# Optimization experiments

Hardware: AMD Instinct MI355X
Metric: run time of the kernel (lower is better)

Reference implementation:

```python
import jax, jax.numpy as jnp
import numpy as np

EPS = 1e-8
LN_EPS = 1e-5


def _norm_no_nan(x, axis=-1, keepdims=False):
    return jnp.sqrt(jnp.clip(jnp.sum(x * x, axis=axis, keepdims=keepdims), EPS))


def gvp_apply(s, v, wh, ws_w, ws_b, wv, use_acts):
    # s: [*, si], v: [*, vi, 3]; activations = (relu, sigmoid) when use_acts
    vt = jnp.swapaxes(v, -1, -2)                        # [*, 3, vi]
    vh = jnp.matmul(vt, wh.T)                           # [*, 3, h]
    vn = _norm_no_nan(vh, axis=-2)                      # [*, h]
    s_out = jnp.matmul(jnp.concatenate([s, vn], -1), ws_w.T) + ws_b
    v_out = jnp.swapaxes(jnp.matmul(vh, wv.T), -1, -2)  # [*, vo, 3]
    if use_acts:
        v_out = v_out * jax.nn.sigmoid(_norm_no_nan(v_out, axis=-1, keepdims=True))
        s_out = jax.nn.relu(s_out)
    return s_out, v_out


def tuple_layernorm(s, v, g, b):
    mu = jnp.mean(s, -1, keepdims=True)
    var = jnp.mean(jnp.square(s - mu), -1, keepdims=True)
    s = (s - mu) / jnp.sqrt(var + LN_EPS) * g + b
    vn2 = jnp.clip(jnp.sum(v * v, -1, keepdims=True), EPS)  # [N, nv, 1]
    v = v / jnp.sqrt(jnp.mean(vn2, -2, keepdims=True))
    return s, v


def gvp_conv_layer(node_s, node_v, edge_s, edge_v, edge_index,
                   msg0_wh, msg0_wsw, msg0_wsb, msg0_wv,
                   msg1_wh, msg1_wsw, msg1_wsb, msg1_wv,
                   msg2_wh, msg2_wsw, msg2_wsb, msg2_wv,
                   ln0_g, ln0_b,
                   ff0_wh, ff0_wsw, ff0_wsb, ff0_wv,
                   ff1_wh, ff1_wsw, ff1_wsb, ff1_wv,
                   ln1_g, ln1_b):
    N = node_s.shape[0]
    src, dst = edge_index[0], edge_index[1]  # PyG: x_j = x[edge_index[0]], x_i = x[edge_index[1]]
    # gather + tuple_cat((s_j, v_j), edge_attr, (s_i, v_i))
    ms = jnp.concatenate([node_s[src], edge_s, node_s[dst]], -1)   # [E, 2*ns+es]
    mv = jnp.concatenate([node_v[src], edge_v, node_v[dst]], -2)   # [E, 2*nv+ev, 3]
    # message function: 3 GVPs, last with no activations
    ms, mv = gvp_apply(ms, mv, msg0_wh, msg0_wsw, msg0_wsb, msg0_wv, True)
    ms, mv = gvp_apply(ms, mv, msg1_wh, msg1_wsw, msg1_wsb, msg1_wv, True)
    ms, mv = gvp_apply(ms, mv, msg2_wh, msg2_wsw, msg2_wsb, msg2_wv, False)
    # mean aggregation over incoming edges per target node
    cnt = jax.ops.segment_sum(jnp.ones_like(ms[:, 0]), dst, num_segments=N)
    denom = jnp.maximum(cnt, 1.0)[:, None]
    agg_s = jax.ops.segment_sum(ms, dst, num_segments=N) / denom
    agg_v = jax.ops.segment_sum(mv, dst, num_segments=N) / denom[..., None]
    # residual + LayerNorm (dropout = identity in eval)
    s, v = tuple_layernorm(node_s + agg_s, node_v + agg_v, ln0_g, ln0_b)
    # feedforward: 2 GVPs, hidden (4*ns, 2*nv), last with no activations
    fs, fv = gvp_apply(s, v, ff0_wh, ff0_wsw, ff0_wsb, ff0_wv, True)
    fs, fv = gvp_apply(fs, fv, ff1_wh, ff1_wsw, ff1_wsb, ff1_wv, False)
    return tuple_layernorm(s + fs, v + fv, ln1_g, ln1_b)


def setup_inputs() -> dict:
    key = jax.random.key(0)
    ks = iter(jax.random.split(key, 64))
    N, E = 10000, 200000
    NS, NV, ES, EV = 128, 32, 32, 1

    def _lin(out_d, in_d):
        return jax.random.normal(next(ks), (out_d, in_d), jnp.float32) / np.float32(np.sqrt(in_d))

    inp = {
        'node_s': jax.random.normal(next(ks), (N, NS), jnp.float32),
        'node_v': jax.random.normal(next(ks), (N, NV, 3), jnp.float32),
        'edge_s': jax.random.normal(next(ks), (E, ES), jnp.float32),
        'edge_v': jax.random.normal(next(ks), (E, EV, 3), jnp.float32),
        'edge_index': jax.random.randint(next(ks), (2, E), 0, N, dtype=jnp.int32),
    }
    si0, vi0 = 2 * NS + ES, 2 * NV + EV            # 288, 65
    h0 = max(vi0, NV)                              # 65
    inp['msg0_wh'] = _lin(h0, vi0)
    inp['msg0_wsw'] = _lin(NS, h0 + si0)
    inp['msg0_wsb'] = jnp.zeros((NS,), jnp.float32)
    inp['msg0_wv'] = _lin(NV, h0)
    for name in ('msg1', 'msg2'):
        inp[name + '_wh'] = _lin(NV, NV)
        inp[name + '_wsw'] = _lin(NS, NV + NS)
        inp[name + '_wsb'] = jnp.zeros((NS,), jnp.float32)
        inp[name + '_wv'] = _lin(NV, NV)
    inp['ln0_g'] = jnp.ones((NS,), jnp.float32)
    inp['ln0_b'] = jnp.zeros((NS,), jnp.float32)
    HS, HV = 4 * NS, 2 * NV                        # 512, 64
    hf0 = max(NV, HV)                              # 64
    inp['ff0_wh'] = _lin(hf0, NV)
    inp['ff0_wsw'] = _lin(HS, hf0 + NS)
    inp['ff0_wsb'] = jnp.zeros((HS,), jnp.float32)
    inp['ff0_wv'] = _lin(HV, hf0)
    hf1 = max(HV, NV)                              # 64
    inp['ff1_wh'] = _lin(hf1, HV)
    inp['ff1_wsw'] = _lin(NS, hf1 + HS)
    inp['ff1_wsb'] = jnp.zeros((NS,), jnp.float32)
    inp['ff1_wv'] = _lin(NV, hf1)
    inp['ln1_g'] = jnp.ones((NS,), jnp.float32)
    inp['ln1_b'] = jnp.zeros((NS,), jnp.float32)
    return inp


def reference(node_s, node_v, edge_s, edge_v, edge_index,
              msg0_wh, msg0_wsw, msg0_wsb, msg0_wv,
              msg1_wh, msg1_wsw, msg1_wsb, msg1_wv,
              msg2_wh, msg2_wsw, msg2_wsb, msg2_wv,
              ln0_g, ln0_b,
              ff0_wh, ff0_wsw, ff0_wsb, ff0_wv,
              ff1_wh, ff1_wsw, ff1_wsb, ff1_wv,
              ln1_g, ln1_b):
    return gvp_conv_layer(node_s, node_v, edge_s, edge_v, edge_index,
                          msg0_wh, msg0_wsw, msg0_wsb, msg0_wv,
                          msg1_wh, msg1_wsw, msg1_wsb, msg1_wv,
                          msg2_wh, msg2_wsw, msg2_wsb, msg2_wv,
                          ln0_g, ln0_b,
                          ff0_wh, ff0_wsw, ff0_wsb, ff0_wv,
                          ff1_wh, ff1_wsw, ff1_wsb, ff1_wv,
                          ln1_g, ln1_b)
```

## Files before the change

kernel.cpp:

```cpp
#include <hip/hip_runtime.h>

typedef unsigned short u16;
typedef __attribute__((ext_vector_type(8))) short bf16x8;
typedef __attribute__((ext_vector_type(4))) float f32x4;

__device__ __forceinline__ float b2f(u16 h){ return __uint_as_float(((unsigned)h)<<16); }
__device__ __forceinline__ u16 f2b(float f){
  unsigned u = __float_as_uint(f);
  unsigned r = ((u>>16)&1u) + 0x7fffu;
  return (u16)((u+r)>>16);
}
__device__ __forceinline__ short4 pack4(float4 f){
  short4 s; s.x=(short)f2b(f.x); s.y=(short)f2b(f.y); s.z=(short)f2b(f.z); s.w=(short)f2b(f.w);
  return s;
}

#define WB0   0
#define WB1   49152
#define WB2   69632
#define WBF0  90112
#define WBF1  188416
#define WB_TOTAL 262144

#define V_WH0   0
#define V_WV0   7680
#define V_WH1   10752
#define V_WV1   11776
#define V_WH2   12800
#define V_WV2   13824
#define NV_FF0H 14848
#define NV_FF0V 16896
#define NV_FF1H 20992
#define NV_FF1V 25088
#define WV_TOTAL 27136

__global__ __launch_bounds__(256) void k_wb(const float* __restrict__ w0,
    const float* __restrict__ w1, const float* __restrict__ w2,
    const float* __restrict__ f0, const float* __restrict__ f1,
    u16* __restrict__ WB){
  int t = blockIdx.x*256 + threadIdx.x;
  if (t < 49152){
    int o = t/384, k = t - o*384;
    WB[WB0 + t] = f2b(k < 353 ? w0[(size_t)o*353 + k] : 0.f);
    return;
  }
  t -= 49152;
  if (t < 20480){ WB[WB1 + t] = f2b(w1[t]); return; }
  t -= 20480;
  if (t < 20480){ WB[WB2 + t] = f2b(w2[t]); return; }
  t -= 20480;
  if (t < 98304){ WB[WBF0 + t] = f2b(f0[t]); return; }
  t -= 98304;
  if (t < 73728){ WB[WBF1 + t] = f2b(f1[t]); return; }
}

__global__ __launch_bounds__(256) void k_wv(const float* __restrict__ wh0, const float* __restrict__ wv0,
    const float* __restrict__ wh1, const float* __restrict__ wv1,
    const float* __restrict__ wh2, const float* __restrict__ wv2,
    const float* __restrict__ nf0h, const float* __restrict__ nf0v,
    const float* __restrict__ nf1h, const float* __restrict__ nf1v,
    u16* __restrict__ WVb){
  int t = blockIdx.x*256 + threadIdx.x;
  if (t < 7680){
    int n=t/96, k=t-n*96;
    float v = 0.f;
    if (n < 65){
      if (k < 32)       v = wh0[(size_t)n*65 + k];
      else if (k < 64)  v = wh0[(size_t)n*65 + 33 + (k-32)];
      else if (k == 64) v = wh0[(size_t)n*65 + 32];
    }
    WVb[V_WH0+t] = f2b(v);
    return;
  }
  t -= 7680;
  if (t < 3072){
    int n=t/96, k=t-n*96;
    WVb[V_WV0+t] = f2b((k<65) ? wv0[(size_t)n*65+k] : 0.f);
    return;
  }
  t -= 3072;
  if (t < 1024){ WVb[V_WH1+t]=f2b(wh1[t]); return; }
  t -= 1024;
  if (t < 1024){ WVb[V_WV1+t]=f2b(wv1[t]); return; }
  t -= 1024;
  if (t < 1024){ WVb[V_WH2+t]=f2b(wh2[t]); return; }
  t -= 1024;
  if (t < 1024){ WVb[V_WV2+t]=f2b(wv2[t]); return; }
  t -= 1024;
  if (t < 2048){ WVb[NV_FF0H+t]=f2b(nf0h[t]); return; }
  t -= 2048;
  if (t < 4096){ WVb[NV_FF0V+t]=f2b(nf0v[t]); return; }
  t -= 4096;
  if (t < 4096){ WVb[NV_FF1H+t]=f2b(nf1h[t]); return; }
  t -= 4096;
  if (t < 2048){ WVb[NV_FF1V+t]=f2b(nf1v[t]); return; }
}

__global__ __launch_bounds__(256) void k_prep(const float* __restrict__ node_s,
    const float* __restrict__ node_v, u16* __restrict__ node_sb,
    u16* __restrict__ node_vb, int N){
  int t = blockIdx.x*256 + threadIdx.x;
  if (t < N*128){ node_sb[t] = f2b(node_s[t]); return; }
  t -= N*128;
  if (t < N*96){
    int n=t/96, r=t-n*96, d=r>>5, vo=r&31;
    node_vb[(size_t)n*96 + d*32 + vo] = f2b(node_v[(size_t)n*96 + vo*3 + d]);
  }
}

__global__ __launch_bounds__(256) void k_hist(const int* __restrict__ ei, int E,
                                              float* __restrict__ cnt){
  int e = blockIdx.x*256 + threadIdx.x;
  if (e < E) atomicAdd(&cnt[ei[(size_t)E + e]], 1.f);
}

__global__ __launch_bounds__(256) void k_scan(const float* __restrict__ cnt,
                                              int* __restrict__ wpos, int N){
  __shared__ int part[256];
  const int tid = threadIdx.x;
  const int per = (N + 255)/256;
  const int base = tid*per;
  int s = 0;
  for (int i=0;i<per;++i){ int n=base+i; if (n<N) s += (int)cnt[n]; }
  part[tid] = s; __syncthreads();
  for (int st=1; st<256; st<<=1){
    int v = (tid>=st) ? part[tid-st] : 0;
    __syncthreads();
    part[tid] += v;
    __syncthreads();
  }
  int run = part[tid] - s;
  for (int i=0;i<per;++i){ int n=base+i; if (n<N){ wpos[n]=run; run += (int)cnt[n]; } }
}

__global__ __launch_bounds__(256) void k_scatter(const int* __restrict__ ei, int E,
                                                 int* __restrict__ wpos, int* __restrict__ perm){
  int e = blockIdx.x*256 + threadIdx.x;
  if (e >= E) return;
  int d = ei[(size_t)E + e];
  int pos = atomicAdd(&wpos[d], 1);
  perm[pos] = e;
}

__global__ __launch_bounds__(256) void k_sortedge(
    const float* __restrict__ es, const float* __restrict__ ev,
    const int* __restrict__ perm,
    u16* __restrict__ esb, u16* __restrict__ evb, int E)
{
  int t = blockIdx.x*256 + threadIdx.x;
  if (t >= E*9) return;
  int pos = t/9, p = t - pos*9;
  int e = perm[pos];
  if (p < 8){
    float4 f = *(const float4*)&es[(size_t)e*32 + 4*p];
    *(short4*)&esb[(size_t)pos*32 + 4*p] = pack4(f);
  } else {
    evb[(size_t)pos*4+0] = f2b(ev[(size_t)e*3+0]);
    evb[(size_t)pos*4+1] = f2b(ev[(size_t)e*3+1]);
    evb[(size_t)pos*4+2] = f2b(ev[(size_t)e*3+2]);
    evb[(size_t)pos*4+3] = 0;
  }
}

#define EPB 32
__global__ __launch_bounds__(512) void k_edge_fused(
    const u16* __restrict__ node_sb, const u16* __restrict__ node_vb,
    const u16* __restrict__ esb, const u16* __restrict__ evb,
    const int* __restrict__ ei, int E, const int* __restrict__ perm,
    const u16* __restrict__ WB, const u16* __restrict__ WVb,
    const float* __restrict__ b0p, const float* __restrict__ b1p, const float* __restrict__ b2p,
    float* __restrict__ agg_s, float* __restrict__ agg_v)
{
  __shared__ __align__(16) char R1[42240];
  __shared__ __align__(16) u16 VN0[EPB][80];
  __shared__ __align__(16) u16 VN1[EPB][32];
  __shared__ __align__(16) u16 VN2[EPB][32];
  __shared__ int SD[EPB][2];
  u16 (*B0)[104]  = (u16(*)[104])R1;
  u16 (*B1)[104]  = (u16(*)[104])(R1 + 20480);
  float (*SCv)[33] = (float(*)[33])R1;
  u16 (*A)[392]   = (u16(*)[392])R1;
  float (*SC)[132] = (float(*)[132])R1;

  const int tid = threadIdx.x;
  const int w = tid>>6, l = tid&63;
  const int le0 = blockIdx.x*EPB;

  if (tid < EPB){
    int le = le0 + tid;
    int ge = (le<E) ? perm[le] : 0;
    SD[tid][0] = ei[ge];
    SD[tid][1] = ei[(size_t)E + ge];
  }
  __syncthreads();
  for (int u=tid; u<96*16; u+=512){
    int r=u>>4, g=u&15, ee=r/3, d=r-ee*3;
    int le=le0+ee;
    short4 v = {0,0,0,0};
    if (le<E){
      int node = (g<8) ? SD[ee][0] : SD[ee][1];
      v = *(const short4*)&node_vb[(size_t)node*96 + d*32 + 4*(g&7)];
    }
    *(short4*)&B0[r][4*g] = v;
  }
  for (int u=tid; u<96*8; u+=512){
    int r=u>>3, g=u&7, ee=r/3, d=r-ee*3;
    int le=le0+ee;
    short4 v = {0,0,0,0};
    if (g==0 && le<E) v.x = (short)evb[(size_t)le*4 + d];
    *(short4*)&B0[r][64+4*g] = v;
  }
  for (int u=tid; u<96*4; u+=512){
    int r=u>>2, g=u&3;
    *(short4*)&B1[r][80+4*g] = (short4){0,0,0,0};
  }
  __syncthreads();

  auto mm = [&](const u16 (*Ai)[104], int woff, int Kp, int NT, u16 (*C)[104]){
    const int nks = Kp>>5;
    for (int t=w; t<6*NT; t+=8){
      int mt = t % 6, nt = t / 6;
      f32x4 acc = {0.f,0.f,0.f,0.f};
      for (int ks=0; ks<nks; ++ks){
        bf16x8 af = *(const bf16x8*)&Ai[mt*16 + (l&15)][ks*32 + (l>>4)*8];
        bf16x8 bf = *(const bf16x8*)&WVb[woff + (size_t)(nt*16 + (l&15))*Kp + ks*32 + (l>>4)*8];
        acc = __builtin_amdgcn_mfma_f32_16x16x32_bf16(af, bf, acc, 0, 0, 0);
      }
      const int col = nt*16 + (l&15);
      const int r0 = mt*16 + (l>>4)*4;
      C[r0+0][col]=f2b(acc[0]); C[r0+1][col]=f2b(acc[1]);
      C[r0+2][col]=f2b(acc[2]); C[r0+3][col]=f2b(acc[3]);
    }
  };

  mm(B0, V_WH0, 96, 5, B1);
  __syncthreads();
  for (int u=tid; u<EPB*80; u+=512){
    int ee=u/80, h=u-ee*80;
    u16 val = 0;
    if (h<65){
      float x0=b2f(B1[ee*3+0][h]), x1=b2f(B1[ee*3+1][h]), x2=b2f(B1[ee*3+2][h]);
      val = f2b(sqrtf(fmaxf(x0*x0+x1*x1+x2*x2, 1e-8f)));
    }
    VN0[ee][h] = val;
  }
  mm(B1, V_WV0, 96, 2, B0);
  __syncthreads();
  for (int u=tid; u<EPB*32; u+=512){
    int ee=u>>5, vo=u&31;
    float x0=b2f(B0[ee*3+0][vo]), x1=b2f(B0[ee*3+1][vo]), x2=b2f(B0[ee*3+2][vo]);
    float nn=sqrtf(fmaxf(x0*x0+x1*x1+x2*x2, 1e-8f));
    float sg=1.f/(1.f+__expf(-nn));
    B0[ee*3+0][vo]=f2b(x0*sg); B0[ee*3+1][vo]=f2b(x1*sg); B0[ee*3+2][vo]=f2b(x2*sg);
  }
  __syncthreads();
  mm(B0, V_WH1, 32, 2, B1);
  __syncthreads();
  for (int u=tid; u<EPB*32; u+=512){
    int ee=u>>5, h=u&31;
    float x0=b2f(B1[ee*3+0][h]), x1=b2f(B1[ee*3+1][h]), x2=b2f(B1[ee*3+2][h]);
    VN1[ee][h] = f2b(sqrtf(fmaxf(x0*x0+x1*x1+x2*x2, 1e-8f)));
  }
  mm(B1, V_WV1, 32, 2, B0);
  __syncthreads();
  for (int u=tid; u<EPB*32; u+=512){
    int ee=u>>5, vo=u&31;
    float x0=b2f(B0[ee*3+0][vo]), x1=b2f(B0[ee*3+1][vo]), x2=b2f(B0[ee*3+2][vo]);
    float nn=sqrtf(fmaxf(x0*x0+x1*x1+x2*x2, 1e-8f));
    float sg=1.f/(1.f+__expf(-nn));
    B0[ee*3+0][vo]=f2b(x0*sg); B0[ee*3+1][vo]=f2b(x1*sg); B0[ee*3+2][vo]=f2b(x2*sg);
  }
  __syncthreads();
  mm(B0, V_WH2, 32, 2, B1);
  __syncthreads();
  for (int u=tid; u<EPB*32; u+=512){
    int ee=u>>5, h=u&31;
    float x0=b2f(B1[ee*3+0][h]), x1=b2f(B1[ee*3+1][h]), x2=b2f(B1[ee*3+2][h]);
    VN2[ee][h] = f2b(sqrtf(fmaxf(x0*x0+x1*x1+x2*x2, 1e-8f)));
  }
  for (int t=w; t<12; t+=8){
    int mt = t % 6, nt = t / 6;
    f32x4 acc = {0.f,0.f,0.f,0.f};
    bf16x8 af = *(const bf16x8*)&B1[mt*16 + (l&15)][(l>>4)*8];
    bf16x8 bf = *(const bf16x8*)&WVb[V_WV2 + (size_t)(nt*16 + (l&15))*32 + (l>>4)*8];
    acc = __builtin_amdgcn_mfma_f32_16x16x32_bf16(af, bf, acc, 0, 0, 0);
    const int vo = nt*16 + (l&15);
    const int r0 = mt*16 + (l>>4)*4;
    #pragma unroll
    for (int j=0;j<4;++j){
      int r = r0 + j;
      int le = le0 + r/3;
      SCv[r][vo] = (le < E) ? acc[j] : 0.f;
    }
  }
  __syncthreads();
  if (tid < 96){
    const int vo = tid & 31, d = tid >> 5;
    float run = 0.f; int prev = -1;
    for (int ee=0; ee<EPB; ++ee){
      int le = le0 + ee;
      int dn = (le<E) ? SD[ee][1] : -1;
      if (dn != prev){
        if (prev >= 0) atomicAdd(&agg_v[(size_t)prev*96 + vo*3 + d], run);
        run = 0.f; prev = dn;
      }
      run += SCv[ee*3+d][vo];
    }
    if (prev >= 0) atomicAdd(&agg_v[(size_t)prev*96 + vo*3 + d], run);
  }
  __syncthreads();

  for (int u=tid; u<EPB*98; u+=512){
    int ee = u/98, g = u - ee*98;
    int le = le0+ee;
    short4 v = {0,0,0,0};
    if (le<E){
      if (g < 32)      v = *(const short4*)&node_sb[(size_t)SD[ee][0]*128 + 4*g];
      else if (g < 40) v = *(const short4*)&esb[(size_t)le*32 + 4*(g-32)];
      else if (g < 72) v = *(const short4*)&node_sb[(size_t)SD[ee][1]*128 + 4*(g-40)];
      else if (g < 92) v = *(const short4*)&VN0[ee][4*(g-72)];
    }
    *(short4*)&A[ee][4*g] = v;
  }
  __syncthreads();

  const int mt = w>>2, nt = w&3;
  const int n_a = nt*32 + (l&15), n_b = n_a + 16;
  const int kq = (l>>4)*8;
  const int ma = mt*16 + (l&15);
  f32x4 ca = {0.f,0.f,0.f,0.f}, cb = {0.f,0.f,0.f,0.f};

  for (int kk=0; kk<384; kk+=32){
    bf16x8 af = *(const bf16x8*)&A[ma][kk + kq];
    bf16x8 b1 = *(const bf16x8*)&WB[WB0 + (size_t)n_a*384 + kk + kq];
    bf16x8 b2 = *(const bf16x8*)&WB[WB0 + (size_t)n_b*384 + kk + kq];
    ca = __builtin_amdgcn_mfma_f32_16x16x32_bf16(af, b1, ca, 0, 0, 0);
    cb = __builtin_amdgcn_mfma_f32_16x16x32_bf16(af, b2, cb, 0, 0, 0);
  }
  __syncthreads();
  {
    float ba = b0p[n_a], bb = b0p[n_b];
    #pragma unroll
    for (int j=0;j<4;++j){
      int r = mt*16 + (l>>4)*4 + j;
      A[r][n_a] = f2b(fmaxf(ca[j] + ba, 0.f));
      A[r][n_b] = f2b(fmaxf(cb[j] + bb, 0.f));
    }
  }
  for (int u=tid; u<EPB*8; u+=512){
    int ee=u>>3, q=u&7;
    *(short4*)&A[ee][128+4*q] = *(const short4*)&VN1[ee][4*q];
  }
  __syncthreads();

  ca = (f32x4){0.f,0.f,0.f,0.f}; cb = (f32x4){0.f,0.f,0.f,0.f};
  for (int kk=0; kk<160; kk+=32){
    bf16x8 af = *(const bf16x8*)&A[ma][kk + kq];
    bf16x8 b1 = *(const bf16x8*)&WB[WB1 + (size_t)n_a*160 + kk + kq];
    bf16x8 b2 = *(const bf16x8*)&WB[WB1 + (size_t)n_b*160 + kk + kq];
    ca = __builtin_amdgcn_mfma_f32_16x16x32_bf16(af, b1, ca, 0, 0, 0);
    cb = __builtin_amdgcn_mfma_f32_16x16x32_bf16(af, b2, cb, 0, 0, 0);
  }
  __syncthreads();
  {
    float ba = b1p[n_a], bb = b1p[n_b];
    #pragma unroll
    for (int j=0;j<4;++j){
      int r = mt*16 + (l>>4)*4 + j;
      A[r][n_a] = f2b(fmaxf(ca[j] + ba, 0.f));
      A[r][n_b] = f2b(fmaxf(cb[j] + bb, 0.f));
    }
  }
  for (int u=tid; u<EPB*8; u+=512){
    int ee=u>>3, q=u&7;
    *(short4*)&A[ee][128+4*q] = *(const short4*)&VN2[ee][4*q];
  }
  __syncthreads();

  ca = (f32x4){0.f,0.f,0.f,0.f}; cb = (f32x4){0.f,0.f,0.f,0.f};
  for (int kk=0; kk<160; kk+=32){
    bf16x8 af = *(const bf16x8*)&A[ma][kk + kq];
    bf16x8 b1 = *(const bf16x8*)&WB[WB2 + (size_t)n_a*160 + kk + kq];
    bf16x8 b2 = *(const bf16x8*)&WB[WB2 + (size_t)n_b*160 + kk + kq];
    ca = __builtin_amdgcn_mfma_f32_16x16x32_bf16(af, b1, ca, 0, 0, 0);
    cb = __builtin_amdgcn_mfma_f32_16x16x32_bf16(af, b2, cb, 0, 0, 0);
  }
  __syncthreads();
  {
    float ba = b2p[n_a], bb = b2p[n_b];
    #pragma unroll
    for (int j=0;j<4;++j){
      int r = mt*16 + (l>>4)*4 + j;
      int le = le0 + r;
      SC[r][n_a] = (le<E) ? (ca[j] + ba) : 0.f;
      SC[r][n_b] = (le<E) ? (cb[j] + bb) : 0.f;
    }
  }
  __syncthreads();
  if (tid < 128){
    const int c = tid;
    float run = 0.f; int prev = -1;
    for (int r=0; r<EPB; ++r){
      int le = le0 + r;
      int dn = (le<E) ? SD[r][1] : -1;
      if (dn != prev){
        if (prev >= 0) atomicAdd(&agg_s[(size_t)prev*128 + c], run);
        run = 0.f; prev = dn;
      }
      run += SC[r][c];
    }
    if (prev >= 0) atomicAdd(&agg_s[(size_t)prev*128 + c], run);
  }
}

__global__ __launch_bounds__(256) void k_ln0(
    const float* __restrict__ node_s, const float* __restrict__ node_v,
    const float* __restrict__ agg_s, const float* __restrict__ agg_v,
    const float* __restrict__ cnt,
    const float* __restrict__ g, const float* __restrict__ b,
    float* __restrict__ s_mid, float* __restrict__ v_mid, int N)
{
  const int tid = threadIdx.x, q = tid&3;
  const int n = blockIdx.x*64 + (tid>>2);
  const bool live = n < N;
  const float inv = live ? 1.f/fmaxf(cnt[n], 1.f) : 1.f;
  float xs[32];
  float sum=0.f, ss=0.f;
  if (live){
    #pragma unroll
    for (int j=0;j<8;++j){
      float4 a = *(const float4*)&node_s[(size_t)n*128 + q*32 + 4*j];
      float4 c = *(const float4*)&agg_s[(size_t)n*128 + q*32 + 4*j];
      xs[4*j+0]=a.x+c.x*inv; xs[4*j+1]=a.y+c.y*inv; xs[4*j+2]=a.z+c.z*inv; xs[4*j+3]=a.w+c.w*inv;
      sum += xs[4*j+0]+xs[4*j+1]+xs[4*j+2]+xs[4*j+3];
      ss  += xs[4*j+0]*xs[4*j+0]+xs[4*j+1]*xs[4*j+1]+xs[4*j+2]*xs[4*j+2]+xs[4*j+3]*xs[4*j+3];
    }
  }
  sum += __shfl_xor(sum,1); sum += __shfl_xor(sum,2);
  ss  += __shfl_xor(ss,1);  ss  += __shfl_xor(ss,2);
  const float mu = sum*(1.f/128.f);
  const float var = fmaxf(ss*(1.f/128.f) - mu*mu, 0.f);
  const float rstd = rsqrtf(var + 1e-5f);
  if (live){
    #pragma unroll
    for (int j=0;j<8;++j){
      float4 gg = *(const float4*)&g[q*32 + 4*j];
      float4 bb = *(const float4*)&b[q*32 + 4*j];
      float4 o;
      o.x=(xs[4*j+0]-mu)*rstd*gg.x+bb.x; o.y=(xs[4*j+1]-mu)*rstd*gg.y+bb.y;
      o.z=(xs[4*j+2]-mu)*rstd*gg.z+bb.z; o.w=(xs[4*j+3]-mu)*rstd*gg.w+bb.w;
      *(float4*)&s_mid[(size_t)n*128 + q*32 + 4*j] = o;
    }
  }
  float yv[24]; float vs=0.f;
  if (live){
    #pragma unroll
    for (int j=0;j<6;++j){
      float4 a = *(const float4*)&node_v[(size_t)n*96 + q*24 + 4*j];
      float4 c = *(const float4*)&agg_v[(size_t)n*96 + q*24 + 4*j];
      yv[4*j+0]=a.x+c.x*inv; yv[4*j+1]=a.y+c.y*inv; yv[4*j+2]=a.z+c.z*inv; yv[4*j+3]=a.w+c.w*inv;
    }
    #pragma unroll
    for (int vv=0; vv<8; ++vv){
      float z0=yv[3*vv], z1=yv[3*vv+1], z2=yv[3*vv+2];
      vs += fmaxf(z0*z0+z1*z1+z2*z2, 1e-8f);
    }
  }
  vs += __shfl_xor(vs,1); vs += __shfl_xor(vs,2);
  const float scale = rsqrtf(vs*(1.f/32.f));
  if (live){
    #pragma unroll
    for (int vv=0; vv<8; ++vv){
      int vo = q*8 + vv;
      v_mid[(size_t)n*96 + vo]      = yv[3*vv]*scale;
      v_mid[(size_t)n*96 + 32 + vo] = yv[3*vv+1]*scale;
      v_mid[(size_t)n*96 + 64 + vo] = yv[3*vv+2]*scale;
    }
  }
}

__global__ __launch_bounds__(256) void k_node_v(
    const float* __restrict__ v_mid, const u16* __restrict__ WVb,
    u16* __restrict__ vn0f, u16* __restrict__ vn1f, float* __restrict__ fv1, int N)
{
  __shared__ __align__(16) u16 B0[96][104];
  __shared__ __align__(16) u16 B1[96][104];
  const int tid = threadIdx.x;
  const int w = tid>>6, l = tid&63;
  const int n0 = blockIdx.x*32;

  for (int u=tid; u<96*8; u+=256){
    int r=u>>3, g=u&7, nd=r/3, d=r-nd*3;
    int n=n0+nd;
    short4 v = {0,0,0,0};
    if (n<N) v = pack4(*(const float4*)&v_mid[(size_t)n*96 + d*32 + 4*g]);
    *(short4*)&B0[r][4*g] = v;
  }
  __syncthreads();

  auto mm = [&](const u16 (*A)[104], int woff, int Kp, int NT, u16 (*C)[104]){
    const int nks = Kp>>5;
    for (int t=w; t<6*NT; t+=4){
      int mt = t % 6, nt = t / 6;
      f32x4 acc = {0.f,0.f,0.f,0.f};
      for (int ks=0; ks<nks; ++ks){
        bf16x8 af = *(const bf16x8*)&A[mt*16 + (l&15)][ks*32 + (l>>4)*8];
        bf16x8 bf = *(const bf16x8*)&WVb[woff + (size_t)(nt*16 + (l&15))*Kp + ks*32 + (l>>4)*8];
        acc = __builtin_amdgcn_mfma_f32_16x16x32_bf16(af, bf, acc, 0, 0, 0);
      }
      const int col = nt*16 + (l&15);
      const int r0 = mt*16 + (l>>4)*4;
      C[r0+0][col]=f2b(acc[0]); C[r0+1][col]=f2b(acc[1]);
      C[r0+2][col]=f2b(acc[2]); C[r0+3][col]=f2b(acc[3]);
    }
  };

  mm(B0, NV_FF0H, 32, 4, B1);
  __syncthreads();
  for (int u=tid; u<32*64; u+=256){
    int nd=u>>6, h=u&63;
    int n=n0+nd;
    if (n<N){
      float x0=b2f(B1[nd*3+0][h]), x1=b2f(B1[nd*3+1][h]), x2=b2f(B1[nd*3+2][h]);
      vn0f[(size_t)n*64+h] = f2b(sqrtf(fmaxf(x0*x0+x1*x1+x2*x2, 1e-8f)));
    }
  }
  mm(B1, NV_FF0V, 64, 4, B0);
  __syncthreads();
  for (int u=tid; u<32*64; u+=256){
    int nd=u>>6, vo=u&63;
    float x0=b2f(B0[nd*3+0][vo]), x1=b2f(B0[nd*3+1][vo]), x2=b2f(B0[nd*3+2][vo]);
    float nn=sqrtf(fmaxf(x0*x0+x1*x1+x2*x2, 1e-8f));
    float sg=1.f/(1.f+__expf(-nn));
    B0[nd*3+0][vo]=f2b(x0*sg); B0[nd*3+1][vo]=f2b(x1*sg); B0[nd*3+2][vo]=f2b(x2*sg);
  }
  __syncthreads();
  mm(B0, NV_FF1H, 64, 4, B1);
  __syncthreads();
  for (int u=tid; u<32*64; u+=256){
    int nd=u>>6, h=u&63;
    int n=n0+nd;
    if (n<N){
      float x0=b2f(B1[nd*3+0][h]), x1=b2f(B1[nd*3+1][h]), x2=b2f(B1[nd*3+2][h]);
      vn1f[(size_t)n*64+h] = f2b(sqrtf(fmaxf(x0*x0+x1*x1+x2*x2, 1e-8f)));
    }
  }
  for (int t=w; t<12; t+=4){
    int mt = t % 6, nt = t / 6;
    f32x4 acc = {0.f,0.f,0.f,0.f};
    for (int ks=0; ks<2; ++ks){
      bf16x8 af = *(const bf16x8*)&B1[mt*16 + (l&15)][ks*32 + (l>>4)*8];
      bf16x8 bf = *(const bf16x8*)&WVb[NV_FF1V + (size_t)(nt*16 + (l&15))*64 + ks*32 + (l>>4)*8];
      acc = __builtin_amdgcn_mfma_f32_16x16x32_bf16(af, bf, acc, 0, 0, 0);
    }
    const int vo = nt*16 + (l&15);
    const int r0 = mt*16 + (l>>4)*4;
    #pragma unroll
    for (int j=0;j<4;++j){
      int r = r0 + j;
      int nd = r/3, d = r - nd*3;
      int n = n0 + nd;
      if (n < N) fv1[(size_t)n*96 + d*32 + vo] = acc[j];
    }
  }
}

__global__ __launch_bounds__(512) void k_node_s(
    const float* __restrict__ s_mid, const u16* __restrict__ vn0f, const u16* __restrict__ vn1f,
    const float* __restrict__ v_mid, const float* __restrict__ fv1,
    const u16* __restrict__ WB,
    const float* __restrict__ fb0, const float* __restrict__ fb1,
    const float* __restrict__ ln1g, const float* __restrict__ ln1b,
    float* __restrict__ out, int N)
{
  __shared__ __align__(16) char U1[16896];
  __shared__ __align__(16) u16 A2[32][584];
  u16 (*A1)[200] = (u16(*)[200])U1;
  float (*FS)[132] = (float(*)[132])U1;
  const int tid = threadIdx.x;
  const int n0 = blockIdx.x*32;

  for (int u=tid; u<32*48; u+=512){
    int nd = u/48, g = u - nd*48;
    int n = n0+nd;
    short4 v = {0,0,0,0};
    if (n<N){
      if (g < 32) v = pack4(*(const float4*)&s_mid[(size_t)n*128 + 4*g]);
      else        v = *(const short4*)&vn0f[(size_t)n*64 + 4*(g-32)];
    }
    *(short4*)&A1[nd][4*g] = v;
  }
  __syncthreads();

  const int w = tid>>6, l = tid&63;
  const int mt = w>>2, ng = w&3;
  const int kq = (l>>4)*8;
  const int ma = mt*16 + (l&15);
  const int r0 = mt*16 + (l>>4)*4;

  for (int nt2=0; nt2<8; ++nt2){
    const int nt = ng*8 + nt2;
    const int col = nt*16 + (l&15);
    f32x4 acc = {0.f,0.f,0.f,0.f};
    for (int ks=0; ks<6; ++ks){
      bf16x8 af = *(const bf16x8*)&A1[ma][ks*32 + kq];
      bf16x8 bf = *(const bf16x8*)&WB[WBF0 + (size_t)col*192 + ks*32 + kq];
      acc = __builtin_amdgcn_mfma_f32_16x16x32_bf16(af, bf, acc, 0, 0, 0);
    }
    float bias = fb0[col];
    #pragma unroll
    for (int j=0;j<4;++j) A2[r0+j][col] = f2b(fmaxf(acc[j] + bias, 0.f));
  }
  __syncthreads();
  for (int u=tid; u<32*16; u+=512){
    int nd=u>>4, q=u&15;
    int n=n0+nd;
    short4 v = {0,0,0,0};
    if (n<N) v = *(const short4*)&vn1f[(size_t)n*64 + 4*q];
    *(short4*)&A2[nd][512+4*q] = v;
  }
  __syncthreads();

  for (int nt2=0; nt2<2; ++nt2){
    const int nt = ng*2 + nt2;
    const int col = nt*16 + (l&15);
    f32x4 acc = {0.f,0.f,0.f,0.f};
    for (int ks=0; ks<18; ++ks){
      bf16x8 af = *(const bf16x8*)&A2[ma][ks*32 + kq];
      bf16x8 bf = *(const bf16x8*)&WB[WBF1 + (size_t)col*576 + ks*32 + kq];
      acc = __builtin_amdgcn_mfma_f32_16x16x32_bf16(af, bf, acc, 0, 0, 0);
    }
    float bias = fb1[col];
    #pragma unroll
    for (int j=0;j<4;++j) FS[r0+j][col] = acc[j] + bias;
  }
  __syncthreads();

  {
    const int nd = tid>>4, q = tid&15;
    const int n = n0 + nd;
    const bool live = n < N;
    float xs[8], sum=0.f, ss=0.f;
    #pragma unroll
    for (int j=0;j<8;++j){
      int c = q*8 + j;
      float x = 0.f;
      if (live) x = s_mid[(size_t)n*128 + c] + FS[nd][c];
      xs[j] = x; sum += x; ss += x*x;
    }
    #pragma unroll
    for (int m=1; m<16; m<<=1){ sum += __shfl_xor(sum, m); ss += __shfl_xor(ss, m); }
    const float mu = sum*(1.f/128.f);
    const float var = fmaxf(ss*(1.f/128.f) - mu*mu, 0.f);
    const float rstd = rsqrtf(var + 1e-5f);
    if (live){
      #pragma unroll
      for (int j=0;j<8;++j){
        int c = q*8 + j;
        out[(size_t)n*128 + c] = (xs[j]-mu)*rstd*ln1g[c] + ln1b[c];
      }
    }
    float z[2][3]; float vs = 0.f;
    #pragma unroll
    for (int j=0;j<2;++j){
      int vo = q + 16*j;
      #pragma unroll
      for (int d=0;d<3;++d){
        float y = live ? (v_mid[(size_t)n*96 + d*32 + vo] + fv1[(size_t)n*96 + d*32 + vo]) : 0.f;
        z[j][d] = y;
      }
      vs += fmaxf(z[j][0]*z[j][0]+z[j][1]*z[j][1]+z[j][2]*z[j][2], 1e-8f);
    }
    #pragma unroll
    for (int m=1; m<16; m<<=1) vs += __shfl_xor(vs, m);
    const float scale = rsqrtf(vs*(1.f/32.f));
    if (live){
      size_t base = (size_t)N*128 + (size_t)n*96;
      #pragma unroll
      for (int j=0;j<2;++j){
        int vo = q + 16*j;
        out[base + vo*3 + 0] = z[j][0]*scale;
        out[base + vo*3 + 1] = z[j][1]*scale;
        out[base + vo*3 + 2] = z[j][2]*scale;
      }
    }
  }
}

extern "C" void kernel_launch(void* const* d_in, const int* in_sizes, int n_in,
                              void* d_out, int out_size, void* d_ws, size_t ws_size,
                              hipStream_t stream)
{
  (void)n_in; (void)out_size; (void)ws_size;
  const int N = in_sizes[0]/128;
  const int E = in_sizes[4]/2;
  const int* ei = (const int*)d_in[4];

  size_t off = 0;
  auto alloc = [&](size_t bytes)->char*{
    size_t o = (off + 255) & ~(size_t)255;
    off = o + bytes;
    return (char*)d_ws + o;
  };
  u16*   WB      = (u16*)alloc((size_t)WB_TOTAL*2);
  u16*   WVb     = (u16*)alloc((size_t)WV_TOTAL*2);
  float* agg_s   = (float*)alloc((size_t)N*128*4);
  float* agg_v   = (float*)alloc((size_t)N*96*4);
  float* cnt     = (float*)alloc((size_t)N*4);
  size_t aggBytes = (size_t)((char*)(cnt+N) - (char*)agg_s);
  float* s_mid   = (float*)alloc((size_t)N*128*4);
  float* v_mid   = (float*)alloc((size_t)N*96*4);
  u16*   node_sb = (u16*)alloc((size_t)N*128*2);
  u16*   node_vb = (u16*)alloc((size_t)N*96*2);
  u16*   vn0f    = (u16*)alloc((size_t)N*64*2);
  u16*   vn1f    = (u16*)alloc((size_t)N*64*2);
  float* fv1     = (float*)alloc((size_t)N*96*4);
  int*   wpos    = (int*)alloc((size_t)N*4);
  int*   perm    = (int*)alloc((size_t)E*4);
  u16*   esb     = (u16*)alloc((size_t)E*32*2);
  u16*   evb     = (u16*)alloc((size_t)E*4*2);

  hipMemsetAsync(agg_s, 0, aggBytes, stream);
  k_wb<<<dim3((WB_TOTAL+255)/256), dim3(256), 0, stream>>>(
      (const float*)d_in[6], (const float*)d_in[10], (const float*)d_in[14],
      (const float*)d_in[20], (const float*)d_in[24], WB);
  k_wv<<<dim3((WV_TOTAL+255)/256), dim3(256), 0, stream>>>(
      (const float*)d_in[5], (const float*)d_in[8], (const float*)d_in[9],
      (const float*)d_in[12], (const float*)d_in[13], (const float*)d_in[16],
      (const float*)d_in[19], (const float*)d_in[22], (const float*)d_in[23],
      (const float*)d_in[26], WVb);
  k_prep<<<dim3((N*224+255)/256), dim3(256), 0, stream>>>(
      (const float*)d_in[0], (const float*)d_in[1], node_sb, node_vb, N);
  k_hist<<<dim3((E+255)/256), dim3(256), 0, stream>>>(ei, E, cnt);
  k_scan<<<dim3(1), dim3(256), 0, stream>>>(cnt, wpos, N);
  k_scatter<<<dim3((E+255)/256), dim3(256), 0, stream>>>(ei, E, wpos, perm);
  k_sortedge<<<dim3(((size_t)E*9+255)/256), dim3(256), 0, stream>>>(
      (const float*)d_in[2], (const float*)d_in[3], perm, esb, evb, E);

  k_edge_fused<<<dim3((E+EPB-1)/EPB), dim3(512), 0, stream>>>(
      node_sb, node_vb, esb, evb, ei, E, perm, WB, WVb,
      (const float*)d_in[7], (const float*)d_in[11], (const float*)d_in[15],
      agg_s, agg_v);

  k_ln0<<<dim3((N+63)/64), dim3(256), 0, stream>>>(
      (const float*)d_in[0], (const float*)d_in[1], agg_s, agg_v, cnt,
      (const float*)d_in[17], (const float*)d_in[18], s_mid, v_mid, N);

  k_node_v<<<dim3((N+31)/32), dim3(256), 0, stream>>>(v_mid, WVb, vn0f, vn1f, fv1, N);
  k_node_s<<<dim3((N+31)/32), dim3(512), 0, stream>>>(
      s_mid, vn0f, vn1f, v_mid, fv1, WB,
      (const float*)d_in[21], (const float*)d_in[25],
      (const float*)d_in[27], (const float*)d_in[28],
      (float*)d_out, N);
}
```

Before: 523.7 us.

## Prefetch scalar gather into registers early; parallelize segmented atomic reductions

The scalar-feature gather for the edge GEMM (source/dest node scalars and edge scalars) is now issued into registers at kernel start and written to shared memory later, so its global-memory latency overlaps the vector GVP stages. The segmented per-destination reductions for agg_v and agg_s are split across four and four thread groups of 8 edges each, which raises parallelism but can issue more atomics. Edge scalars are also converted to bf16 linearly in the prep kernel so the sort kernel only moves bf16 data. This adds register pressure from five prefetched short4 values per thread and an extra buffer pass.

```diff
diff --git a/kernel.cpp b/kernel.cpp
--- a/kernel.cpp
+++ b/kernel.cpp
@@ -97,15 +97,19 @@
 }
 
 __global__ __launch_bounds__(256) void k_prep(const float* __restrict__ node_s,
-    const float* __restrict__ node_v, u16* __restrict__ node_sb,
-    u16* __restrict__ node_vb, int N){
+    const float* __restrict__ node_v, const float* __restrict__ edge_s,
+    u16* __restrict__ node_sb, u16* __restrict__ node_vb, u16* __restrict__ esb_lin,
+    int N, int E){
   int t = blockIdx.x*256 + threadIdx.x;
   if (t < N*128){ node_sb[t] = f2b(node_s[t]); return; }
   t -= N*128;
   if (t < N*96){
     int n=t/96, r=t-n*96, d=r>>5, vo=r&31;
     node_vb[(size_t)n*96 + d*32 + vo] = f2b(node_v[(size_t)n*96 + vo*3 + d]);
-  }
+    return;
+  }
+  t -= N*96;
+  if (t < E*32){ esb_lin[t] = f2b(edge_s[t]); return; }
 }
 
 __global__ __launch_bounds__(256) void k_hist(const int* __restrict__ ei, int E,
@@ -143,7 +147,7 @@
 }
 
 __global__ __launch_bounds__(256) void k_sortedge(
-    const float* __restrict__ es, const float* __restrict__ ev,
+    const u16* __restrict__ esb_lin, const float* __restrict__ ev,
     const int* __restrict__ perm,
     u16* __restrict__ esb, u16* __restrict__ evb, int E)
 {
@@ -152,8 +156,7 @@
   int pos = t/9, p = t - pos*9;
   int e = perm[pos];
   if (p < 8){
-    float4 f = *(const float4*)&es[(size_t)e*32 + 4*p];
-    *(short4*)&esb[(size_t)pos*32 + 4*p] = pack4(f);
+    *(short4*)&esb[(size_t)pos*32 + 4*p] = *(const short4*)&esb_lin[(size_t)e*32 + 4*p];
   } else {
     evb[(size_t)pos*4+0] = f2b(ev[(size_t)e*3+0]);
     evb[(size_t)pos*4+1] = f2b(ev[(size_t)e*3+1]);
@@ -193,6 +196,27 @@
     SD[tid][1] = ei[(size_t)E + ge];
   }
   __syncthreads();
+
+  short4 pre0={0,0,0,0}, pre1={0,0,0,0}, pre2={0,0,0,0}, pre3={0,0,0,0}, pre4={0,0,0,0};
+  {
+    auto ld = [&](int u)->short4{
+      short4 v = {0,0,0,0};
+      if (u < EPB*72){
+        int ee = u/72, g = u - ee*72;
+        int le = le0+ee;
+        if (le<E){
+          if (g < 32)      v = *(const short4*)&node_sb[(size_t)SD[ee][0]*128 + 4*g];
+          else if (g < 40) v = *(const short4*)&esb[(size_t)le*32 + 4*(g-32)];
+          else             v = *(const short4*)&node_sb[(size_t)SD[ee][1]*128 + 4*(g-40)];
+        }
+      }
+      return v;
+    };
+    pre0 = ld(tid);          pre1 = ld(tid + 512);
+    pre2 = ld(tid + 1024);   pre3 = ld(tid + 1536);
+    pre4 = ld(tid + 2048);
+  }
+
   for (int u=tid; u<96*16; u+=512){
     int r=u>>4, g=u&15, ee=r/3, d=r-ee*3;
     int le=le0+ee;
@@ -294,10 +318,11 @@
     }
   }
   __syncthreads();
-  if (tid < 96){
-    const int vo = tid & 31, d = tid >> 5;
+  if (tid < 384){
+    const int part = tid / 96, vd = tid - part*96;
+    const int vo = vd & 31, d = vd >> 5;
     float run = 0.f; int prev = -1;
-    for (int ee=0; ee<EPB; ++ee){
+    for (int ee=part*8; ee<part*8+8; ++ee){
       int le = le0 + ee;
       int dn = (le<E) ? SD[ee][1] : -1;
       if (dn != prev){
@@ -310,16 +335,19 @@
   }
   __syncthreads();
 
-  for (int u=tid; u<EPB*98; u+=512){
-    int ee = u/98, g = u - ee*98;
-    int le = le0+ee;
+  {
+    auto st = [&](int u, short4 v){
+      if (u < EPB*72){
+        int ee = u/72, g = u - ee*72;
+        *(short4*)&A[ee][4*g] = v;
+      }
+    };
+    st(tid, pre0); st(tid+512, pre1); st(tid+1024, pre2); st(tid+1536, pre3); st(tid+2048, pre4);
+  }
+  for (int u=tid; u<EPB*26; u+=512){
+    int ee = u/26, g = 72 + (u - ee*26);
     short4 v = {0,0,0,0};
-    if (le<E){
-      if (g < 32)      v = *(const short4*)&node_sb[(size_t)SD[ee][0]*128 + 4*g];
-      else if (g < 40) v = *(const short4*)&esb[(size_t)le*32 + 4*(g-32)];
-      else if (g < 72) v = *(const short4*)&node_sb[(size_t)SD[ee][1]*128 + 4*(g-40)];
-      else if (g < 92) v = *(const short4*)&VN0[ee][4*(g-72)];
-    }
+    if (g < 92) v = *(const short4*)&VN0[ee][4*(g-72)];
     *(short4*)&A[ee][4*g] = v;
   }
   __syncthreads();
@@ -397,10 +425,10 @@
     }
   }
   __syncthreads();
-  if (tid < 128){
-    const int c = tid;
+  {
+    const int part = tid >> 7, c = tid & 127;
     float run = 0.f; int prev = -1;
-    for (int r=0; r<EPB; ++r){
+    for (int r=part*8; r<part*8+8; ++r){
       int le = le0 + r;
       int dn = (le<E) ? SD[r][1] : -1;
       if (dn != prev){
@@ -717,6 +745,7 @@
   float* fv1     = (float*)alloc((size_t)N*96*4);
   int*   wpos    = (int*)alloc((size_t)N*4);
   int*   perm    = (int*)alloc((size_t)E*4);
+  u16*   esb_lin = (u16*)alloc((size_t)E*32*2);
   u16*   esb     = (u16*)alloc((size_t)E*32*2);
   u16*   evb     = (u16*)alloc((size_t)E*4*2);
 
@@ -729,13 +758,14 @@
       (const float*)d_in[12], (const float*)d_in[13], (const float*)d_in[16],
       (const float*)d_in[19], (const float*)d_in[22], (const float*)d_in[23],
       (const float*)d_in[26], WVb);
-  k_prep<<<dim3((N*224+255)/256), dim3(256), 0, stream>>>(
-      (const float*)d_in[0], (const float*)d_in[1], node_sb, node_vb, N);
+  k_prep<<<dim3(((size_t)N*224 + (size_t)E*32 + 255)/256), dim3(256), 0, stream>>>(
+      (const float*)d_in[0], (const float*)d_in[1], (const float*)d_in[2],
+      node_sb, node_vb, esb_lin, N, E);
   k_hist<<<dim3((E+255)/256), dim3(256), 0, stream>>>(ei, E, cnt);
   k_scan<<<dim3(1), dim3(256), 0, stream>>>(cnt, wpos, N);
   k_scatter<<<dim3((E+255)/256), dim3(256), 0, stream>>>(ei, E, wpos, perm);
   k_sortedge<<<dim3(((size_t)E*9+255)/256), dim3(256), 0, stream>>>(
-      (const float*)d_in[2], (const float*)d_in[3], perm, esb, evb, E);
+      esb_lin, (const float*)d_in[3], perm, esb, evb, E);
 
   k_edge_fused<<<dim3((E+EPB-1)/EPB), dim3(512), 0, stream>>>(
       node_sb, node_vb, esb, evb, ei, E, perm, WB, WVb,
```

Result: faster. 504.9 us (median of 2 runs) (-3.6%).
